# Performance work log

Measured on AMD Instinct MI355X. Metric: run time of the kernel, lower is better.

## Reference

```python
import jax, jax.numpy as jnp
import numpy as np

N_NODES = 100000
N_EDGES = 1600000
IN_CH = 32
HID = 128
OUT_CH = 32


def _glorot(key, shape):
    fan_in, fan_out = shape[1], shape[0]
    lim = (6.0 / (fan_in + fan_out)) ** 0.5
    return jax.random.uniform(key, shape, jnp.float32, -lim, lim)


def setup_inputs() -> dict:
    key = jax.random.key(0)
    ks = jax.random.split(key, 8)
    x = jax.random.normal(ks[0], (N_NODES, IN_CH), jnp.float32)
    edge_index = jax.random.randint(ks[1], (2, N_EDGES), 0, N_NODES, jnp.int64)
    # SAGEConv params: lin_l (neighbor agg, with bias), lin_r (root, no bias)
    W1_l = _glorot(ks[2], (HID, IN_CH))
    W1_r = _glorot(ks[3], (HID, IN_CH))
    b1 = jnp.zeros((HID,), jnp.float32)
    W2_l = _glorot(ks[4], (OUT_CH, HID))
    W2_r = _glorot(ks[5], (OUT_CH, HID))
    b2 = jnp.zeros((OUT_CH,), jnp.float32)
    return {"x": x, "edge_index": edge_index,
            "W1_l": W1_l, "W1_r": W1_r, "b1": b1,
            "W2_l": W2_l, "W2_r": W2_r, "b2": b2}


def _sage_conv(x, src, dst, W_l, W_r, b):
    # mean aggregation of neighbor features j -> i over edges (src=j, dst=i)
    agg = jax.ops.segment_sum(x[src], dst, num_segments=N_NODES)  # [N, C]
    deg = jax.ops.segment_sum(jnp.ones((src.shape[0],), x.dtype), dst,
                              num_segments=N_NODES)
    agg = agg / jnp.maximum(deg, 1.0)[:, None]
    return agg @ W_l.T + x @ W_r.T + b


def reference(x, edge_index, W1_l, W1_r, b1, W2_l, W2_r, b2):
    src, dst = edge_index[0], edge_index[1]
    h = _sage_conv(x, src, dst, W1_l, W1_r, b1)
    h = jax.nn.relu(h)
    # dropout is identity in eval mode (training=False)
    out = _sage_conv(h, src, dst, W2_l, W2_r, b2)
    return out
```

## Files before the change

### kernel.cpp

```cpp
#include <hip/hip_runtime.h>
#include <hip/hip_bf16.h>

typedef __hip_bfloat16 bf16;
typedef unsigned short ush;
typedef __attribute__((ext_vector_type(8))) unsigned short ush8;
typedef __attribute__((ext_vector_type(8))) short s8v;
typedef __attribute__((ext_vector_type(4))) float f4;

#define IN_CH 32
#define HID 128
#define OUT_CH 32
#define S_CAP 32
#define OVF_CAP 80000
#define NB_MAX 2048
#define SC_CHUNK 8192

__device__ __forceinline__ float bf2f(ush u) {
    return __uint_as_float(((unsigned)u) << 16);
}
__device__ __forceinline__ ush f2bf(float f) {
    __hip_bfloat16 b = __float2bfloat16(f);
    return __builtin_bit_cast(ush, b);
}
__device__ __forceinline__ float ldf(const void* __restrict__ p, size_t idx, int isbf16) {
    return isbf16 ? bf2f(((const ush*)p)[idx]) : ((const float*)p)[idx];
}
__device__ __forceinline__ int ld_edge(const int* __restrict__ ei, size_t elem, int wide) {
    return wide ? ei[2 * elem] : ei[elem];
}

__global__ void k_detect(const unsigned short* __restrict__ xraw,
                         const int* __restrict__ ei, int* __restrict__ flags) {
    __shared__ int cnt_exp, any_nz;
    if (threadIdx.x == 0) { cnt_exp = 0; any_nz = 0; }
    __syncthreads();
    int local = 0;
    for (int k = threadIdx.x; k < 4096; k += 256) {
        int e = (xraw[k] >> 7) & 0xFF;
        if (e >= 100 && e <= 140) ++local;
    }
    atomicAdd(&cnt_exp, local);
    for (int k = threadIdx.x; k < 2048; k += 256)
        if (ei[2 * k + 1] != 0) any_nz = 1;
    __syncthreads();
    if (threadIdx.x == 0) {
        flags[0] = (cnt_exp > 3500) ? 1 : 0;
        flags[1] = any_nz ? 0 : 1;
    }
}

__global__ void k_fillp(const int* __restrict__ ei, int n_edges,
                        const int* __restrict__ flags,
                        int* __restrict__ cnt, int* __restrict__ csr,
                        int* __restrict__ ovf, int* __restrict__ ovfn) {
    int e = blockIdx.x * blockDim.x + threadIdx.x;
    if (e >= n_edges) return;
    int w = flags[1];
    int d  = ld_edge(ei, (size_t)n_edges + e, w);
    int sc = ld_edge(ei, (size_t)e, w);
    int r = atomicAdd(&cnt[d], 1);
    if (r < S_CAP) {
        csr[d * S_CAP + r] = sc;
    } else {
        int o = atomicAdd(ovfn, 1);
        if (o < OVF_CAP) { ((int2*)ovf)[o] = make_int2(d, sc); }
    }
}


__global__ __launch_bounds__(256) void k_hist(
        const int* __restrict__ ei, int n_edges,
        const int* __restrict__ flags,
        int* __restrict__ hist, int NB) {
    __shared__ int hl[NB_MAX];
    int t = threadIdx.x;
    for (int k = t; k < NB; k += 256) hl[k] = 0;
    __syncthreads();
    int w = flags[1];
    int stride = gridDim.x * 256;
    for (int e = blockIdx.x * 256 + t; e < n_edges; e += stride) {
        int d = ld_edge(ei, (size_t)n_edges + e, w);
        atomicAdd(&hl[d >> 8], 1);
    }
    __syncthreads();
    for (int k = t; k < NB; k += 256)
        if (hl[k]) atomicAdd(&hist[k], hl[k]);
}

__global__ __launch_bounds__(256) void k_scan(
        const int* __restrict__ hist,
        int* __restrict__ base, int* __restrict__ cursor, int NB) {
    __shared__ int part[256];
    int t = threadIdx.x;
    int chunk = (NB + 255) / 256;
    int lo = t * chunk, hi = min(NB, (t + 1) * chunk);
    int s = 0;
    for (int k = lo; k < hi; ++k) s += hist[k];
    part[t] = s;
    __syncthreads();
    if (t == 0) {
        int r = 0;
        for (int q = 0; q < 256; ++q) { int v = part[q]; part[q] = r; r += v; }
        base[NB] = r;
    }
    __syncthreads();
    int r = part[t];
    for (int k = lo; k < hi; ++k) {
        base[k] = r; cursor[k] = r;
        r += hist[k];
    }
}

__global__ __launch_bounds__(256) void k_scatter(
        const int* __restrict__ ei, int n_edges,
        const int* __restrict__ flags,
        int* __restrict__ cursor, int* __restrict__ pairs, int NB) {
    __shared__ int cA[NB_MAX];
    __shared__ int oA[NB_MAX];
    int t = threadIdx.x;
    int w = flags[1];
    int e0 = blockIdx.x * SC_CHUNK;
    int ecnt = min(SC_CHUNK, n_edges - e0);
    if (ecnt <= 0) return;
    for (int k = t; k < NB; k += 256) cA[k] = 0;
    __syncthreads();
    for (int k = t; k < ecnt; k += 256) {
        int d = ld_edge(ei, (size_t)n_edges + e0 + k, w);
        atomicAdd(&cA[d >> 8], 1);
    }
    __syncthreads();
    for (int b = t; b < NB; b += 256) {
        int c = cA[b];
        oA[b] = c ? atomicAdd(&cursor[b], c) : 0;
        cA[b] = 0;
    }
    __syncthreads();
    for (int k = t; k < ecnt; k += 256) {
        int d  = ld_edge(ei, (size_t)n_edges + e0 + k, w);
        int sc = ld_edge(ei, (size_t)e0 + k, w);
        int b = d >> 8;
        int r = atomicAdd(&cA[b], 1);
        pairs[oA[b] + r] = sc | ((d & 255) << 24);
    }
}

__global__ __launch_bounds__(256) void k_build(
        const int* __restrict__ pairs, const int* __restrict__ base,
        int* __restrict__ cnt, int* __restrict__ csr,
        int* __restrict__ ovf, int* __restrict__ ovfn, int n_nodes) {
    __shared__ int cntL[256];
    __shared__ int im[256 * S_CAP];
    int b = blockIdx.x;
    int t = threadIdx.x;
    cntL[t] = 0;
    __syncthreads();
    int s0 = base[b], s1 = base[b + 1];
    int node0 = b << 8;
    for (int k = s0 + t; k < s1; k += 256) {
        int v = pairs[k];
        int src = v & 0x00FFFFFF;
        int ld = ((unsigned)v) >> 24;
        int r = atomicAdd(&cntL[ld], 1);
        if (r < S_CAP) {
            im[ld * S_CAP + r] = src;
        } else {
            int o = atomicAdd(ovfn, 1);
            if (o < OVF_CAP) { ((int2*)ovf)[o] = make_int2(node0 + ld, src); }
        }
    }
    __syncthreads();
    int nvalid = min(256, n_nodes - node0);
    if (t < nvalid) cnt[node0 + t] = cntL[t];
    for (int k = t; k < nvalid * S_CAP; k += 256)
        csr[(size_t)node0 * S_CAP + k] = im[k];
}

__global__ __launch_bounds__(256, 8) void k_agg1(
        const void* __restrict__ x,
        const int* __restrict__ cnt, const int* __restrict__ csr,
        const int* __restrict__ ovf, const int* __restrict__ ovfn,
        const int* __restrict__ flags,
        ush* __restrict__ aggb, int n_nodes) {
    int fb = flags[0];
    int t = threadIdx.x;
    int wave = t >> 6, lane = t & 63;
    int g4 = lane & 60;
    int c  = lane & 3;
    int node = (blockIdx.x * 4 + wave) * 16 + (lane >> 2);
    bool valid = node < n_nodes;
    int nd = valid ? node : n_nodes - 1;
    int dg = cnt[nd];
    int lim = min(dg, S_CAP);
    int idxr[8];
    {
        int4 i0 = *(const int4*)&csr[(size_t)nd * S_CAP + c * 8];
        int4 i1 = *(const int4*)&csr[(size_t)nd * S_CAP + c * 8 + 4];
        idxr[0] = i0.x; idxr[1] = i0.y; idxr[2] = i0.z; idxr[3] = i0.w;
        idxr[4] = i1.x; idxr[5] = i1.y; idxr[6] = i1.z; idxr[7] = i1.w;
    }
    int lmax = lim;
    lmax = max(lmax, __shfl_xor(lmax, 4));
    lmax = max(lmax, __shfl_xor(lmax, 8));
    lmax = max(lmax, __shfl_xor(lmax, 16));
    lmax = max(lmax, __shfl_xor(lmax, 32));
    float acc[8] = {0, 0, 0, 0, 0, 0, 0, 0};
    if (fb) {
        const ush* xb = (const ush*)x;
        for (int kb = 0; kb < 4; ++kb) {
            if (kb * 8 >= lmax) break;
#pragma unroll
            for (int kk = 0; kk < 8; ++kk) {
                int src = __shfl(idxr[kk], g4 + kb);
                if (kb * 8 + kk < lim) {
                    ush8 v = *(const ush8*)(xb + (size_t)src * IN_CH + c * 8);
#pragma unroll
                    for (int j = 0; j < 8; ++j) acc[j] += bf2f(v[j]);
                }
            }
        }
        if (dg > S_CAP) {
            int on = min(*ovfn, OVF_CAP);
            for (int k = 0; k < on; ++k) {
                int2 pr = ((const int2*)ovf)[k];
                if (pr.x == nd && valid) {
                    ush8 v = *(const ush8*)(xb + (size_t)pr.y * IN_CH + c * 8);
#pragma unroll
                    for (int j = 0; j < 8; ++j) acc[j] += bf2f(v[j]);
                }
            }
        }
    } else {
        const float* xb = (const float*)x;
        for (int kb = 0; kb < 4; ++kb) {
            if (kb * 8 >= lmax) break;
#pragma unroll
            for (int kk = 0; kk < 8; ++kk) {
                int src = __shfl(idxr[kk], g4 + kb);
                if (kb * 8 + kk < lim) {
                    const float* rp = xb + (size_t)src * IN_CH + c * 8;
                    f4 a0 = *(const f4*)rp;
                    f4 a1 = *(const f4*)(rp + 4);
#pragma unroll
                    for (int j = 0; j < 4; ++j) { acc[j] += a0[j]; acc[4 + j] += a1[j]; }
                }
            }
        }
        if (dg > S_CAP) {
            int on = min(*ovfn, OVF_CAP);
            for (int k = 0; k < on; ++k) {
                int2 pr = ((const int2*)ovf)[k];
                if (pr.x == nd && valid) {
                    const float* rp = xb + (size_t)pr.y * IN_CH + c * 8;
                    f4 a0 = *(const f4*)rp;
                    f4 a1 = *(const f4*)(rp + 4);
#pragma unroll
                    for (int j = 0; j < 4; ++j) { acc[j] += a0[j]; acc[4 + j] += a1[j]; }
                }
            }
        }
    }
    if (valid) {
        float rd = 1.0f / (float)(dg > 1 ? dg : 1);
        ush8 ov;
#pragma unroll
        for (int j = 0; j < 8; ++j) ov[j] = f2bf(acc[j] * rd);
        *(ush8*)(aggb + (size_t)node * IN_CH + c * 8) = ov;
    }
}

__global__ __launch_bounds__(256, 4) void k_mm1_mfma(
        const void* __restrict__ x, const ush* __restrict__ aggb,
        const void* __restrict__ W1l, const void* __restrict__ W1r,
        const void* __restrict__ b1,
        const int* __restrict__ flags,
        ush* __restrict__ hout, int n_nodes) {
    __shared__ ush wst[HID * 64];
    int fb = flags[0];
    int t = threadIdx.x;
    for (int idx = t; idx < HID * IN_CH; idx += 256) {
        int o = idx >> 5, c = idx & 31;
        wst[o * 64 + c]      = f2bf(ldf(W1l, idx, fb));
        wst[o * 64 + 32 + c] = f2bf(ldf(W1r, idx, fb));
    }
    __syncthreads();
    int wave = t >> 6, lane = t & 63;
    int col  = lane & 15;
    int kgrp = lane >> 4;
    s8v bfr[8][2];
    float bias[8];
#pragma unroll
    for (int tt = 0; tt < 8; ++tt) {
        int o = tt * 16 + col;
#pragma unroll
        for (int q = 0; q < 2; ++q)
            bfr[tt][q] = __builtin_bit_cast(s8v, *(const ush8*)&wst[o * 64 + q * 32 + kgrp * 8]);
        bias[tt] = ldf(b1, o, fb);
    }
    int gw = blockIdx.x * 4 + wave;
    int nw = gridDim.x * 4;
    for (int n0 = gw * 16; n0 < n_nodes; n0 += nw * 16) {
        int arow = n0 + col;
        if (arow >= n_nodes) arow = n_nodes - 1;
        s8v a0 = __builtin_bit_cast(s8v, *(const ush8*)(aggb + (size_t)arow * IN_CH + kgrp * 8));
        s8v a1;
        if (fb) {
            a1 = __builtin_bit_cast(s8v, *(const ush8*)((const ush*)x + (size_t)arow * IN_CH + kgrp * 8));
        } else {
            const float* rp = (const float*)x + (size_t)arow * IN_CH + kgrp * 8;
            f4 v0 = *(const f4*)rp;
            f4 v1 = *(const f4*)(rp + 4);
            ush8 tmp;
#pragma unroll
            for (int j = 0; j < 4; ++j) { tmp[j] = f2bf(v0[j]); tmp[4 + j] = f2bf(v1[j]); }
            a1 = __builtin_bit_cast(s8v, tmp);
        }
        f4 acc[8];
#pragma unroll
        for (int tt = 0; tt < 8; ++tt) {
            f4 z = {0, 0, 0, 0};
            z = __builtin_amdgcn_mfma_f32_16x16x32_bf16(a0, bfr[tt][0], z, 0, 0, 0);
            z = __builtin_amdgcn_mfma_f32_16x16x32_bf16(a1, bfr[tt][1], z, 0, 0, 0);
            acc[tt] = z;
        }
#pragma unroll
        for (int r = 0; r < 4; ++r) {
            int node = n0 + kgrp * 4 + r;
            if (node < n_nodes) {
#pragma unroll
                for (int tt = 0; tt < 8; ++tt) {
                    float v = acc[tt][r] + bias[tt];
                    hout[(size_t)node * HID + tt * 16 + col] = f2bf(v > 0.0f ? v : 0.0f);
                }
            }
        }
    }
}

__global__ __launch_bounds__(256, 4) void k_g_mfma(
        ush* __restrict__ h, ush* __restrict__ gout,
        ush* __restrict__ sb, int sdense,
        const void* __restrict__ W2l, const void* __restrict__ W2r,
        const void* __restrict__ b2,
        const int* __restrict__ flags, int n_nodes) {
    __shared__ ush wst[2 * OUT_CH * HID];
    int fb = flags[0];
    int t = threadIdx.x;
    for (int idx = t; idx < OUT_CH * HID; idx += 256) {
        wst[idx]                  = f2bf(ldf(W2l, idx, fb));
        wst[OUT_CH * HID + idx]   = f2bf(ldf(W2r, idx, fb));
    }
    __syncthreads();
    int wave = t >> 6, lane = t & 63;
    int col  = lane & 15;
    int kgrp = lane >> 4;
    s8v bfr[4][4];
#pragma unroll
    for (int tt = 0; tt < 4; ++tt) {
        int base = (tt < 2 ? 0 : OUT_CH * HID) + ((tt & 1) * 16 + col) * HID + kgrp * 8;
#pragma unroll
        for (int q = 0; q < 4; ++q)
            bfr[tt][q] = __builtin_bit_cast(s8v, *(const ush8*)&wst[base + q * 32]);
    }
    float bias0 = ldf(b2, col, fb);
    float bias1 = ldf(b2, 16 + col, fb);
    int gw = blockIdx.x * 4 + wave;
    int nw = gridDim.x * 4;
    for (int n0 = gw * 16; n0 < n_nodes; n0 += nw * 16) {
        int arow = n0 + col;
        if (arow >= n_nodes) arow = n_nodes - 1;
        const ush* hp = h + (size_t)arow * HID + kgrp * 8;
        s8v a0 = __builtin_bit_cast(s8v, *(const ush8*)(hp));
        s8v a1 = __builtin_bit_cast(s8v, *(const ush8*)(hp + 32));
        s8v a2 = __builtin_bit_cast(s8v, *(const ush8*)(hp + 64));
        s8v a3 = __builtin_bit_cast(s8v, *(const ush8*)(hp + 96));
        f4 acc0 = {0, 0, 0, 0}, acc1 = {0, 0, 0, 0}, acc2 = {0, 0, 0, 0}, acc3 = {0, 0, 0, 0};
        acc0 = __builtin_amdgcn_mfma_f32_16x16x32_bf16(a0, bfr[0][0], acc0, 0, 0, 0);
        acc0 = __builtin_amdgcn_mfma_f32_16x16x32_bf16(a1, bfr[0][1], acc0, 0, 0, 0);
        acc0 = __builtin_amdgcn_mfma_f32_16x16x32_bf16(a2, bfr[0][2], acc0, 0, 0, 0);
        acc0 = __builtin_amdgcn_mfma_f32_16x16x32_bf16(a3, bfr[0][3], acc0, 0, 0, 0);
        acc1 = __builtin_amdgcn_mfma_f32_16x16x32_bf16(a0, bfr[1][0], acc1, 0, 0, 0);
        acc1 = __builtin_amdgcn_mfma_f32_16x16x32_bf16(a1, bfr[1][1], acc1, 0, 0, 0);
        acc1 = __builtin_amdgcn_mfma_f32_16x16x32_bf16(a2, bfr[1][2], acc1, 0, 0, 0);
        acc1 = __builtin_amdgcn_mfma_f32_16x16x32_bf16(a3, bfr[1][3], acc1, 0, 0, 0);
        acc2 = __builtin_amdgcn_mfma_f32_16x16x32_bf16(a0, bfr[2][0], acc2, 0, 0, 0);
        acc2 = __builtin_amdgcn_mfma_f32_16x16x32_bf16(a1, bfr[2][1], acc2, 0, 0, 0);
        acc2 = __builtin_amdgcn_mfma_f32_16x16x32_bf16(a2, bfr[2][2], acc2, 0, 0, 0);
        acc2 = __builtin_amdgcn_mfma_f32_16x16x32_bf16(a3, bfr[2][3], acc2, 0, 0, 0);
        acc3 = __builtin_amdgcn_mfma_f32_16x16x32_bf16(a0, bfr[3][0], acc3, 0, 0, 0);
        acc3 = __builtin_amdgcn_mfma_f32_16x16x32_bf16(a1, bfr[3][1], acc3, 0, 0, 0);
        acc3 = __builtin_amdgcn_mfma_f32_16x16x32_bf16(a2, bfr[3][2], acc3, 0, 0, 0);
        acc3 = __builtin_amdgcn_mfma_f32_16x16x32_bf16(a3, bfr[3][3], acc3, 0, 0, 0);
#pragma unroll
        for (int r = 0; r < 4; ++r) {
            int node = n0 + kgrp * 4 + r;
            if (node < n_nodes) {
                gout[(size_t)node * OUT_CH + col]      = f2bf(acc0[r]);
                gout[(size_t)node * OUT_CH + 16 + col] = f2bf(acc1[r]);
                if (sdense) {
                    sb[(size_t)node * OUT_CH + col]      = f2bf(acc2[r] + bias0);
                    sb[(size_t)node * OUT_CH + 16 + col] = f2bf(acc3[r] + bias1);
                } else {
                    h[(size_t)node * HID + 32 + col]     = f2bf(acc2[r] + bias0);
                    h[(size_t)node * HID + 48 + col]     = f2bf(acc3[r] + bias1);
                }
            }
        }
    }
}

__global__ __launch_bounds__(256, 8) void k_l2g(
        const ush* __restrict__ gbuf, const ush* __restrict__ hs,
        const ush* __restrict__ sb, int sdense,
        const int* __restrict__ cnt, const int* __restrict__ csr,
        const int* __restrict__ ovf, const int* __restrict__ ovfn,
        const int* __restrict__ flags,
        void* __restrict__ out, int n_nodes) {
    int fb = flags[0];
    int t = threadIdx.x;
    int wave = t >> 6, lane = t & 63;
    int g4 = lane & 60;
    int c  = lane & 3;
    int node = (blockIdx.x * 4 + wave) * 16 + (lane >> 2);
    bool valid = node < n_nodes;
    int nd = valid ? node : n_nodes - 1;
    int dg = cnt[nd];
    int lim = min(dg, S_CAP);
    int idxr[8];
    {
        int4 i0 = *(const int4*)&csr[(size_t)nd * S_CAP + c * 8];
        int4 i1 = *(const int4*)&csr[(size_t)nd * S_CAP + c * 8 + 4];
        idxr[0] = i0.x; idxr[1] = i0.y; idxr[2] = i0.z; idxr[3] = i0.w;
        idxr[4] = i1.x; idxr[5] = i1.y; idxr[6] = i1.z; idxr[7] = i1.w;
    }
    int lmax = lim;
    lmax = max(lmax, __shfl_xor(lmax, 4));
    lmax = max(lmax, __shfl_xor(lmax, 8));
    lmax = max(lmax, __shfl_xor(lmax, 16));
    lmax = max(lmax, __shfl_xor(lmax, 32));
    float acc[8] = {0, 0, 0, 0, 0, 0, 0, 0};
    for (int kb = 0; kb < 4; ++kb) {
        if (kb * 8 >= lmax) break;
#pragma unroll
        for (int kk = 0; kk < 8; ++kk) {
            int src = __shfl(idxr[kk], g4 + kb);
            if (kb * 8 + kk < lim) {
                ush8 v = *(const ush8*)(gbuf + (size_t)src * OUT_CH + c * 8);
#pragma unroll
                for (int j = 0; j < 8; ++j) acc[j] += bf2f(v[j]);
            }
        }
    }
    if (dg > S_CAP) {
        int on = min(*ovfn, OVF_CAP);
        for (int k = 0; k < on; ++k) {
            int2 pr = ((const int2*)ovf)[k];
            if (pr.x == nd && valid) {
                ush8 v = *(const ush8*)(gbuf + (size_t)pr.y * OUT_CH + c * 8);
#pragma unroll
                for (int j = 0; j < 8; ++j) acc[j] += bf2f(v[j]);
            }
        }
    }
    if (valid) {
        float rd = 1.0f / (float)(dg > 1 ? dg : 1);
        ush8 selfv = sdense
            ? *(const ush8*)(sb + (size_t)node * OUT_CH + c * 8)
            : *(const ush8*)(hs + (size_t)node * HID + 32 + c * 8);
        if (fb) {
            ush8 ov;
#pragma unroll
            for (int j = 0; j < 8; ++j)
                ov[j] = f2bf(acc[j] * rd + bf2f(selfv[j]));
            *(ush8*)((ush*)out + (size_t)node * OUT_CH + c * 8) = ov;
        } else {
            float* op = (float*)out + (size_t)node * OUT_CH + c * 8;
            f4 a0, a1;
#pragma unroll
            for (int j = 0; j < 4; ++j) {
                a0[j] = acc[j] * rd + bf2f(selfv[j]);
                a1[j] = acc[4 + j] * rd + bf2f(selfv[4 + j]);
            }
            *(f4*)op = a0;
            *(f4*)(op + 4) = a1;
        }
    }
}

extern "C" void kernel_launch(void* const* d_in, const int* in_sizes, int n_in,
                              void* d_out, int out_size, void* d_ws, size_t ws_size,
                              hipStream_t stream) {
    const void* x   = d_in[0];
    const int*  ei  = (const int*)d_in[1];
    const void* W1l = d_in[2];
    const void* W1r = d_in[3];
    const void* b1  = d_in[4];
    const void* W2l = d_in[5];
    const void* W2r = d_in[6];
    const void* b2  = d_in[7];

    int n_nodes = in_sizes[0] / IN_CH;
    int n_edges = in_sizes[1] / 2;

    char* ws = (char*)d_ws;
    size_t o_cnt = 256;
    size_t o_csr = (o_cnt + (size_t)n_nodes * 4 + 127) & ~(size_t)127;
    size_t o_ovf = (o_csr + ((size_t)n_nodes * S_CAP + 64) * 4 + 127) & ~(size_t)127;
    size_t o_hist = o_ovf + (size_t)OVF_CAP * 8;
    size_t o_h   = (o_hist + (size_t)(3 * (NB_MAX + 2)) * 4 + 255) & ~(size_t)255;
    size_t o_gb  = (o_h + (size_t)n_nodes * HID * 2 + 255) & ~(size_t)255;
    size_t o_ag  = (o_gb + (size_t)n_nodes * OUT_CH * 2 + 255) & ~(size_t)255;
    size_t o_sb  = (o_ag + (size_t)n_nodes * IN_CH * 2 + 255) & ~(size_t)255;
    size_t need_agg = o_ag + (size_t)n_nodes * IN_CH * 2;
    size_t need_sd  = o_sb + (size_t)n_nodes * OUT_CH * 2;

    int* flags = (int*)ws;
    int* ovfn  = (int*)(ws + 128);
    int* cnt   = (int*)(ws + o_cnt);
    int* csr   = (int*)(ws + o_csr);
    int* ovf   = (int*)(ws + o_ovf);
    int* hist  = (int*)(ws + o_hist);
    int* base  = hist + NB_MAX;
    int* curs  = base + NB_MAX + 1;
    ush* h     = (ush*)(ws + o_h);
    int* pairs = (int*)(ws + o_h);
    ush* gbuf  = (ush*)(ws + o_gb);

    ush* aggb  = (ws_size >= need_agg) ? (ush*)(ws + o_ag) : gbuf;
    int  sdense = (ws_size >= need_sd) ? 1 : 0;
    ush* sbuf  = (ush*)(ws + o_sb);

    int NB = (n_nodes + 255) >> 8;
    int use_bucket = (NB <= NB_MAX) && (n_nodes < (1 << 24)) &&
                     ((size_t)n_edges * 4 <= (size_t)n_nodes * HID * 2) && (n_edges > 0);

    hipMemsetAsync(ws, 0, 256, stream);

    k_detect<<<1, 256, 0, stream>>>((const unsigned short*)x, ei, flags);

    if (use_bucket) {
        hipMemsetAsync(hist, 0, (size_t)NB * 4, stream);
        int nchunks = (n_edges + SC_CHUNK - 1) / SC_CHUNK;
        k_hist<<<256, 256, 0, stream>>>(ei, n_edges, flags, hist, NB);
        k_scan<<<1, 256, 0, stream>>>(hist, base, curs, NB);
        k_scatter<<<nchunks, 256, 0, stream>>>(ei, n_edges, flags, curs, pairs, NB);
        k_build<<<NB, 256, 0, stream>>>(pairs, base, cnt, csr, ovf, ovfn, n_nodes);
    } else {
        hipMemsetAsync(cnt, 0, (size_t)n_nodes * 4, stream);
        k_fillp<<<(n_edges + 255) / 256, 256, 0, stream>>>(ei, n_edges, flags, cnt, csr, ovf, ovfn);
    }

    int nblk_g = (n_nodes + 63) / 64;
    k_agg1<<<nblk_g, 256, 0, stream>>>(x, cnt, csr, ovf, ovfn, flags, aggb, n_nodes);
    k_mm1_mfma<<<1024, 256, 0, stream>>>(x, aggb, W1l, W1r, b1, flags, h, n_nodes);
    k_g_mfma<<<1024, 256, 0, stream>>>(h, gbuf, sbuf, sdense, W2l, W2r, b2, flags, n_nodes);
    k_l2g<<<nblk_g, 256, 0, stream>>>(gbuf, h, sbuf, sdense, cnt, csr, ovf, ovfn, flags, d_out, n_nodes);
}
```

Before: 232.6 us.

## Fuse layer-1 matmul and layer-2 projection via per-wave LDS tile

Merges the layer-1 MFMA kernel and the layer-2 projection kernel into one. The hidden activations for each 16-node tile are staged in a padded per-wave LDS tile instead of a global round trip, and the layer-2 inputs are read back from there. This removes the global write and re-read of the 128-wide hidden tensor plus one launch. In exchange it raises register and LDS use (launch bounds drop to 2 blocks per CU, grid 768) and relies on a wave-local lgkmcnt wait instead of a barrier.

```diff
diff --git a/kernel.cpp b/kernel.cpp
--- a/kernel.cpp
+++ b/kernel.cpp
@@ -14,6 +14,7 @@
 #define OVF_CAP 80000
 #define NB_MAX 2048
 #define SC_CHUNK 8192
+#define HT_STRIDE 132
 
 __device__ __forceinline__ float bf2f(ush u) {
     return __uint_as_float(((unsigned)u) << 16);
@@ -268,34 +269,52 @@
     }
 }
 
-__global__ __launch_bounds__(256, 4) void k_mm1_mfma(
+__global__ __launch_bounds__(256, 2) void k_fused(
         const void* __restrict__ x, const ush* __restrict__ aggb,
         const void* __restrict__ W1l, const void* __restrict__ W1r,
         const void* __restrict__ b1,
+        const void* __restrict__ W2l, const void* __restrict__ W2r,
+        const void* __restrict__ b2,
         const int* __restrict__ flags,
-        ush* __restrict__ hout, int n_nodes) {
-    __shared__ ush wst[HID * 64];
+        ush* __restrict__ gout, ush* __restrict__ sb, int sdense,
+        ush* __restrict__ hglob, int n_nodes) {
+    __shared__ ush w1st[HID * 64];
+    __shared__ ush w2st[2 * OUT_CH * HID];
+    __shared__ ush htile[4][16 * HT_STRIDE];
     int fb = flags[0];
     int t = threadIdx.x;
     for (int idx = t; idx < HID * IN_CH; idx += 256) {
         int o = idx >> 5, c = idx & 31;
-        wst[o * 64 + c]      = f2bf(ldf(W1l, idx, fb));
-        wst[o * 64 + 32 + c] = f2bf(ldf(W1r, idx, fb));
+        w1st[o * 64 + c]      = f2bf(ldf(W1l, idx, fb));
+        w1st[o * 64 + 32 + c] = f2bf(ldf(W1r, idx, fb));
+        w2st[idx]                 = f2bf(ldf(W2l, idx, fb));
+        w2st[OUT_CH * HID + idx]  = f2bf(ldf(W2r, idx, fb));
     }
     __syncthreads();
     int wave = t >> 6, lane = t & 63;
     int col  = lane & 15;
     int kgrp = lane >> 4;
-    s8v bfr[8][2];
-    float bias[8];
+    s8v b1fr[8][2];
+    float bs1[8];
 #pragma unroll
     for (int tt = 0; tt < 8; ++tt) {
         int o = tt * 16 + col;
 #pragma unroll
         for (int q = 0; q < 2; ++q)
-            bfr[tt][q] = __builtin_bit_cast(s8v, *(const ush8*)&wst[o * 64 + q * 32 + kgrp * 8]);
-        bias[tt] = ldf(b1, o, fb);
-    }
+            b1fr[tt][q] = __builtin_bit_cast(s8v, *(const ush8*)&w1st[o * 64 + q * 32 + kgrp * 8]);
+        bs1[tt] = ldf(b1, o, fb);
+    }
+    s8v b2fr[4][4];
+#pragma unroll
+    for (int tt = 0; tt < 4; ++tt) {
+        int base = (tt < 2 ? 0 : OUT_CH * HID) + ((tt & 1) * 16 + col) * HID + kgrp * 8;
+#pragma unroll
+        for (int q = 0; q < 4; ++q)
+            b2fr[tt][q] = __builtin_bit_cast(s8v, *(const ush8*)&w2st[base + q * 32]);
+    }
+    float bs2_0 = ldf(b2, col, fb);
+    float bs2_1 = ldf(b2, 16 + col, fb);
+    ush* ht = &htile[wave][0];
     int gw = blockIdx.x * 4 + wave;
     int nw = gridDim.x * 4;
     for (int n0 = gw * 16; n0 < n_nodes; n0 += nw * 16) {
@@ -314,82 +333,44 @@
             for (int j = 0; j < 4; ++j) { tmp[j] = f2bf(v0[j]); tmp[4 + j] = f2bf(v1[j]); }
             a1 = __builtin_bit_cast(s8v, tmp);
         }
-        f4 acc[8];
+        f4 hacc[8];
 #pragma unroll
         for (int tt = 0; tt < 8; ++tt) {
             f4 z = {0, 0, 0, 0};
-            z = __builtin_amdgcn_mfma_f32_16x16x32_bf16(a0, bfr[tt][0], z, 0, 0, 0);
-            z = __builtin_amdgcn_mfma_f32_16x16x32_bf16(a1, bfr[tt][1], z, 0, 0, 0);
-            acc[tt] = z;
+            z = __builtin_amdgcn_mfma_f32_16x16x32_bf16(a0, b1fr[tt][0], z, 0, 0, 0);
+            z = __builtin_amdgcn_mfma_f32_16x16x32_bf16(a1, b1fr[tt][1], z, 0, 0, 0);
+            hacc[tt] = z;
         }
 #pragma unroll
         for (int r = 0; r < 4; ++r) {
-            int node = n0 + kgrp * 4 + r;
-            if (node < n_nodes) {
-#pragma unroll
-                for (int tt = 0; tt < 8; ++tt) {
-                    float v = acc[tt][r] + bias[tt];
-                    hout[(size_t)node * HID + tt * 16 + col] = f2bf(v > 0.0f ? v : 0.0f);
-                }
-            }
-        }
-    }
-}
-
-__global__ __launch_bounds__(256, 4) void k_g_mfma(
-        ush* __restrict__ h, ush* __restrict__ gout,
-        ush* __restrict__ sb, int sdense,
-        const void* __restrict__ W2l, const void* __restrict__ W2r,
-        const void* __restrict__ b2,
-        const int* __restrict__ flags, int n_nodes) {
-    __shared__ ush wst[2 * OUT_CH * HID];
-    int fb = flags[0];
-    int t = threadIdx.x;
-    for (int idx = t; idx < OUT_CH * HID; idx += 256) {
-        wst[idx]                  = f2bf(ldf(W2l, idx, fb));
-        wst[OUT_CH * HID + idx]   = f2bf(ldf(W2r, idx, fb));
-    }
-    __syncthreads();
-    int wave = t >> 6, lane = t & 63;
-    int col  = lane & 15;
-    int kgrp = lane >> 4;
-    s8v bfr[4][4];
-#pragma unroll
-    for (int tt = 0; tt < 4; ++tt) {
-        int base = (tt < 2 ? 0 : OUT_CH * HID) + ((tt & 1) * 16 + col) * HID + kgrp * 8;
-#pragma unroll
-        for (int q = 0; q < 4; ++q)
-            bfr[tt][q] = __builtin_bit_cast(s8v, *(const ush8*)&wst[base + q * 32]);
-    }
-    float bias0 = ldf(b2, col, fb);
-    float bias1 = ldf(b2, 16 + col, fb);
-    int gw = blockIdx.x * 4 + wave;
-    int nw = gridDim.x * 4;
-    for (int n0 = gw * 16; n0 < n_nodes; n0 += nw * 16) {
-        int arow = n0 + col;
-        if (arow >= n_nodes) arow = n_nodes - 1;
-        const ush* hp = h + (size_t)arow * HID + kgrp * 8;
-        s8v a0 = __builtin_bit_cast(s8v, *(const ush8*)(hp));
-        s8v a1 = __builtin_bit_cast(s8v, *(const ush8*)(hp + 32));
-        s8v a2 = __builtin_bit_cast(s8v, *(const ush8*)(hp + 64));
-        s8v a3 = __builtin_bit_cast(s8v, *(const ush8*)(hp + 96));
+#pragma unroll
+            for (int tt = 0; tt < 8; ++tt) {
+                float v = hacc[tt][r] + bs1[tt];
+                ht[(kgrp * 4 + r) * HT_STRIDE + tt * 16 + col] = f2bf(v > 0.0f ? v : 0.0f);
+            }
+        }
+        asm volatile("s_waitcnt lgkmcnt(0)" ::: "memory");
+        s8v A0 = __builtin_bit_cast(s8v, *(const ush8*)&ht[col * HT_STRIDE + 0 * 32 + kgrp * 8]);
+        s8v A1 = __builtin_bit_cast(s8v, *(const ush8*)&ht[col * HT_STRIDE + 1 * 32 + kgrp * 8]);
+        s8v A2 = __builtin_bit_cast(s8v, *(const ush8*)&ht[col * HT_STRIDE + 2 * 32 + kgrp * 8]);
+        s8v A3 = __builtin_bit_cast(s8v, *(const ush8*)&ht[col * HT_STRIDE + 3 * 32 + kgrp * 8]);
         f4 acc0 = {0, 0, 0, 0}, acc1 = {0, 0, 0, 0}, acc2 = {0, 0, 0, 0}, acc3 = {0, 0, 0, 0};
-        acc0 = __builtin_amdgcn_mfma_f32_16x16x32_bf16(a0, bfr[0][0], acc0, 0, 0, 0);
-        acc0 = __builtin_amdgcn_mfma_f32_16x16x32_bf16(a1, bfr[0][1], acc0, 0, 0, 0);
-        acc0 = __builtin_amdgcn_mfma_f32_16x16x32_bf16(a2, bfr[0][2], acc0, 0, 0, 0);
-        acc0 = __builtin_amdgcn_mfma_f32_16x16x32_bf16(a3, bfr[0][3], acc0, 0, 0, 0);
-        acc1 = __builtin_amdgcn_mfma_f32_16x16x32_bf16(a0, bfr[1][0], acc1, 0, 0, 0);
-        acc1 = __builtin_amdgcn_mfma_f32_16x16x32_bf16(a1, bfr[1][1], acc1, 0, 0, 0);
-        acc1 = __builtin_amdgcn_mfma_f32_16x16x32_bf16(a2, bfr[1][2], acc1, 0, 0, 0);
-        acc1 = __builtin_amdgcn_mfma_f32_16x16x32_bf16(a3, bfr[1][3], acc1, 0, 0, 0);
-        acc2 = __builtin_amdgcn_mfma_f32_16x16x32_bf16(a0, bfr[2][0], acc2, 0, 0, 0);
-        acc2 = __builtin_amdgcn_mfma_f32_16x16x32_bf16(a1, bfr[2][1], acc2, 0, 0, 0);
-        acc2 = __builtin_amdgcn_mfma_f32_16x16x32_bf16(a2, bfr[2][2], acc2, 0, 0, 0);
-        acc2 = __builtin_amdgcn_mfma_f32_16x16x32_bf16(a3, bfr[2][3], acc2, 0, 0, 0);
-        acc3 = __builtin_amdgcn_mfma_f32_16x16x32_bf16(a0, bfr[3][0], acc3, 0, 0, 0);
-        acc3 = __builtin_amdgcn_mfma_f32_16x16x32_bf16(a1, bfr[3][1], acc3, 0, 0, 0);
-        acc3 = __builtin_amdgcn_mfma_f32_16x16x32_bf16(a2, bfr[3][2], acc3, 0, 0, 0);
-        acc3 = __builtin_amdgcn_mfma_f32_16x16x32_bf16(a3, bfr[3][3], acc3, 0, 0, 0);
+        acc0 = __builtin_amdgcn_mfma_f32_16x16x32_bf16(A0, b2fr[0][0], acc0, 0, 0, 0);
+        acc0 = __builtin_amdgcn_mfma_f32_16x16x32_bf16(A1, b2fr[0][1], acc0, 0, 0, 0);
+        acc0 = __builtin_amdgcn_mfma_f32_16x16x32_bf16(A2, b2fr[0][2], acc0, 0, 0, 0);
+        acc0 = __builtin_amdgcn_mfma_f32_16x16x32_bf16(A3, b2fr[0][3], acc0, 0, 0, 0);
+        acc1 = __builtin_amdgcn_mfma_f32_16x16x32_bf16(A0, b2fr[1][0], acc1, 0, 0, 0);
+        acc1 = __builtin_amdgcn_mfma_f32_16x16x32_bf16(A1, b2fr[1][1], acc1, 0, 0, 0);
+        acc1 = __builtin_amdgcn_mfma_f32_16x16x32_bf16(A2, b2fr[1][2], acc1, 0, 0, 0);
+        acc1 = __builtin_amdgcn_mfma_f32_16x16x32_bf16(A3, b2fr[1][3], acc1, 0, 0, 0);
+        acc2 = __builtin_amdgcn_mfma_f32_16x16x32_bf16(A0, b2fr[2][0], acc2, 0, 0, 0);
+        acc2 = __builtin_amdgcn_mfma_f32_16x16x32_bf16(A1, b2fr[2][1], acc2, 0, 0, 0);
+        acc2 = __builtin_amdgcn_mfma_f32_16x16x32_bf16(A2, b2fr[2][2], acc2, 0, 0, 0);
+        acc2 = __builtin_amdgcn_mfma_f32_16x16x32_bf16(A3, b2fr[2][3], acc2, 0, 0, 0);
+        acc3 = __builtin_amdgcn_mfma_f32_16x16x32_bf16(A0, b2fr[3][0], acc3, 0, 0, 0);
+        acc3 = __builtin_amdgcn_mfma_f32_16x16x32_bf16(A1, b2fr[3][1], acc3, 0, 0, 0);
+        acc3 = __builtin_amdgcn_mfma_f32_16x16x32_bf16(A2, b2fr[3][2], acc3, 0, 0, 0);
+        acc3 = __builtin_amdgcn_mfma_f32_16x16x32_bf16(A3, b2fr[3][3], acc3, 0, 0, 0);
 #pragma unroll
         for (int r = 0; r < 4; ++r) {
             int node = n0 + kgrp * 4 + r;
@@ -397,11 +378,11 @@
                 gout[(size_t)node * OUT_CH + col]      = f2bf(acc0[r]);
                 gout[(size_t)node * OUT_CH + 16 + col] = f2bf(acc1[r]);
                 if (sdense) {
-                    sb[(size_t)node * OUT_CH + col]      = f2bf(acc2[r] + bias0);
-                    sb[(size_t)node * OUT_CH + 16 + col] = f2bf(acc3[r] + bias1);
+                    sb[(size_t)node * OUT_CH + col]      = f2bf(acc2[r] + bs2_0);
+                    sb[(size_t)node * OUT_CH + 16 + col] = f2bf(acc3[r] + bs2_1);
                 } else {
-                    h[(size_t)node * HID + 32 + col]     = f2bf(acc2[r] + bias0);
-                    h[(size_t)node * HID + 48 + col]     = f2bf(acc3[r] + bias1);
+                    hglob[(size_t)node * HID + 32 + col] = f2bf(acc2[r] + bs2_0);
+                    hglob[(size_t)node * HID + 48 + col] = f2bf(acc3[r] + bs2_1);
                 }
             }
         }
@@ -551,7 +532,7 @@
 
     int nblk_g = (n_nodes + 63) / 64;
     k_agg1<<<nblk_g, 256, 0, stream>>>(x, cnt, csr, ovf, ovfn, flags, aggb, n_nodes);
-    k_mm1_mfma<<<1024, 256, 0, stream>>>(x, aggb, W1l, W1r, b1, flags, h, n_nodes);
-    k_g_mfma<<<1024, 256, 0, stream>>>(h, gbuf, sbuf, sdense, W2l, W2r, b2, flags, n_nodes);
+    k_fused<<<768, 256, 0, stream>>>(x, aggb, W1l, W1r, b1, W2l, W2r, b2, flags,
+                                     gbuf, sbuf, sdense, h, n_nodes);
     k_l2g<<<nblk_g, 256, 0, stream>>>(gbuf, h, sbuf, sdense, cnt, csr, ovf, ovfn, flags, d_out, n_nodes);
 }
```

Result: no change. 236.4 us (+1.6%).
